# Optimization experiments

Hardware: AMD Instinct MI355X
Metric: run time of the kernel (lower is better)

## Reference

```python
import jax, jax.numpy as jnp
import numpy as np

B, L, K, D, S = 8, 1024, 1024, 128, 16  # batch, nodes, eigvecs, d_model(=d_inner), d_state
ABAR_EPS = 1e-3
BN_EPS = 1e-5


def setup_inputs() -> dict:
    key = jax.random.key(0)
    ks = jax.random.split(key, 10)
    x = jax.random.normal(ks[0], (B, L, D), jnp.float32)
    attn_mask = jnp.ones((B, L), jnp.bool_)
    EigVecs = jax.random.normal(ks[1], (B, L, K), jnp.float32)
    EigVals = jax.random.uniform(ks[2], (B, K), jnp.float32)
    # BatchNorm1d (eval mode) params
    bn_gamma = jnp.ones((D,), jnp.float32)
    bn_beta = jnp.zeros((D,), jnp.float32)
    bn_mean = jnp.zeros((D,), jnp.float32)
    bn_var = jnp.ones((D,), jnp.float32)
    # in_proj Linear(D, 2*D)
    W_in = jax.random.normal(ks[3], (D, 2 * D), jnp.float32) / np.float32(np.sqrt(D))
    b_in = jnp.zeros((2 * D,), jnp.float32)
    # SSM params
    log_Delta = np.float32(np.log(1e-3)) + np.float32(np.log(0.1) - np.log(1e-3)) * jax.random.uniform(ks[4], (1, D), jnp.float32)
    Bp = 0.01 * jax.random.normal(ks[5], (1, D, S), jnp.float32)
    Cp = 0.01 * jax.random.normal(ks[6], (1, D, S), jnp.float32)
    log_A_real = jnp.log(0.5 * jnp.ones((D, S), jnp.float32))
    A_imag = jnp.pi * jnp.broadcast_to(jnp.arange(D, dtype=jnp.float32)[:, None], (D, S))
    # out_proj Linear(D, D)
    W_out = jax.random.normal(ks[7], (D, D), jnp.float32) / np.float32(np.sqrt(D))
    b_out = jnp.zeros((D,), jnp.float32)
    return {
        "x": x, "attn_mask": attn_mask, "EigVecs": EigVecs, "EigVals": EigVals,
        "bn_gamma": bn_gamma, "bn_beta": bn_beta, "bn_mean": bn_mean, "bn_var": bn_var,
        "W_in": W_in, "b_in": b_in, "log_Delta": log_Delta, "Bp": Bp, "Cp": Cp,
        "log_A_real": log_A_real, "A_imag": A_imag, "W_out": W_out, "b_out": b_out,
    }


def reference(x, attn_mask, EigVecs, EigVals, bn_gamma, bn_beta, bn_mean, bn_var,
              W_in, b_in, log_Delta, Bp, Cp, log_A_real, A_imag, W_out, b_out):
    # --- eig preprocessing ---
    ev = 1.0 - EigVals[:, :, None, None]            # (B,K,1,1)
    ev = jnp.nan_to_num(ev)
    Q = jnp.nan_to_num(EigVecs)                      # (B,L,K)
    Q = Q / jnp.linalg.norm(Q, axis=-1, keepdims=True)
    Q = jnp.nan_to_num(Q)
    # --- in_proj: BatchNorm1d (eval) + Linear ---
    xb = (x - bn_mean) * (bn_gamma / jnp.sqrt(bn_var + BN_EPS)) + bn_beta
    h = xb @ W_in + b_in                             # (B,L,2D)
    x1, z = jnp.split(h, 2, axis=-1)                 # split [d_model, d_model]
    u = x1 * jax.nn.silu(z)                          # (B,L,D)
    # --- discretized SSM params ---
    delta = jnp.exp(log_Delta)                       # (1,D)
    A = -jnp.exp(log_A_real) + 1j * A_imag           # (D,S) complex
    Abar = jnp.exp(-ABAR_EPS + delta[..., None] * A) # (1,D,S) complex
    Bbar = delta[..., None] * Bp                     # (1,D,S)
    # --- graph Fourier transform ---
    QTX = jnp.einsum('blk,bld->bkd', Q, u)           # (B,K,D)
    QTXB = QTX[..., None] * Bbar                     # (B,K,D,S)
    lamA = ev * Abar[:, None]                        # (B,K,D,S) complex
    lamQ = jnp.real(lamA / (1.0 - lamA) * QTXB)      # A_complex & not BC_complex -> .real
    # --- inverse transform + C reduction (fused) ---
    yssm = jnp.einsum('blk,bkds,ds->bld', Q, lamQ, Cp[0])  # (B,L,D)
    y = jax.nn.silu(yssm) @ W_out + b_out
    return y
```

## Files before the change

kernel.cpp:

```cpp
#include <hip/hip_runtime.h>
#include <math.h>

#define B_ 8
#define L_ 1024
#define K_ 1024
#define D_ 128
#define S_ 16
#define DS_ (D_ * S_)
#define NIT_ 16

typedef short bf16x8 __attribute__((ext_vector_type(8)));
typedef float f32x4 __attribute__((ext_vector_type(4)));
typedef __attribute__((address_space(1))) const unsigned int gu32;
typedef __attribute__((address_space(3))) unsigned int lu32;

__device__ inline unsigned short f2bf(float f) {
    unsigned int u = __float_as_uint(f);
    u = (u + 0x7fffu + ((u >> 16) & 1u)) >> 16;
    return (unsigned short)u;
}
__device__ inline float bf2f(unsigned short h) {
    return __uint_as_float(((unsigned int)h) << 16);
}

__device__ inline size_t bswz(int b, int c, int n) {
    return ((((size_t)b * 32 + (c >> 5)) * 4 + ((c >> 3) & 3)) * 128 + n) * 8;
}

__global__ __launch_bounds__(256) void k_pre(
    const float* __restrict__ E, const float* __restrict__ x,
    const float* __restrict__ g, const float* __restrict__ beta,
    const float* __restrict__ mean, const float* __restrict__ var,
    const float* __restrict__ W_in, const float* __restrict__ b_in,
    const float* __restrict__ log_Delta, const float* __restrict__ Bp,
    const float* __restrict__ Cp, const float* __restrict__ log_A_real,
    const float* __restrict__ A_imag,
    float* __restrict__ rn_out, float* __restrict__ par,
    unsigned short* __restrict__ uswH, unsigned short* __restrict__ uswL) {
    __shared__ float xb[16][128];
    __shared__ float rsum[16];
    __shared__ float rnS[16];
    int bx = blockIdx.x;
    int row0 = bx * 16;
    int t = threadIdx.x;
    if (bx < 8) {
        int i = bx * 256 + t;
        int d = i >> 4, s = i & 15;
        double delta = exp((double)log_Delta[d]);
        double Are = -exp((double)log_A_real[i]);
        double Aim = (double)A_imag[i];
        double mag = exp(-1e-3 + delta * Are);
        double ang = delta * Aim;
        int o = s * D_ + d;
        par[o]           = (float)(mag * cos(ang));
        par[DS_ + o]     = (float)(mag * sin(ang));
        par[2 * DS_ + o] = (float)(delta * (double)Bp[i] * (double)Cp[i]);
    }
    {
        int r = t >> 4, tt = t & 15;
        const float4* Ep = (const float4*)(E + (size_t)(row0 + r) * K_);
        float s = 0.f;
        #pragma unroll
        for (int i = 0; i < 16; ++i) {
            float4 v = Ep[tt + i * 16];
            s += v.x * v.x + v.y * v.y + v.z * v.z + v.w * v.w;
        }
        s += __shfl_xor(s, 8, 64);
        s += __shfl_xor(s, 4, 64);
        s += __shfl_xor(s, 2, 64);
        s += __shfl_xor(s, 1, 64);
        if (tt == 0) rsum[r] = s;
    }
    #pragma unroll
    for (int p = 0; p < 8; ++p) {
        int idx = t + p * 256;
        int dd = idx & 127, r = idx >> 7;
        float sc = g[dd] / sqrtf(var[dd] + 1e-5f);
        xb[r][dd] = (x[(size_t)(row0 + r) * D_ + dd] - mean[dd]) * sc + beta[dd];
    }
    __syncthreads();
    if (t < 16) {
        float rv = 1.0f / sqrtf(rsum[t]);
        rnS[t] = rv;
        rn_out[row0 + t] = rv;
    }
    __syncthreads();
    int j = t & 127, half = t >> 7;
    float acc1[8], acc2[8];
    #pragma unroll
    for (int r = 0; r < 8; ++r) { acc1[r] = 0.f; acc2[r] = 0.f; }
    #pragma unroll 4
    for (int dd = 0; dd < 128; ++dd) {
        float w1 = W_in[dd * 256 + j];
        float w2 = W_in[dd * 256 + 128 + j];
        #pragma unroll
        for (int r = 0; r < 8; ++r) {
            float xv = xb[half * 8 + r][dd];
            acc1[r] = fmaf(xv, w1, acc1[r]);
            acc2[r] = fmaf(xv, w2, acc2[r]);
        }
    }
    float b1 = b_in[j], b2 = b_in[128 + j];
    bf16x8 hv, lv;
    #pragma unroll
    for (int r = 0; r < 8; ++r) {
        int rr = half * 8 + r;
        float x1 = acc1[r] + b1;
        float z  = acc2[r] + b2;
        float sig = 1.0f / (1.0f + __expf(-z));
        float uv = rnS[rr] * x1 * z * sig;
        unsigned short h = f2bf(uv);
        hv[r] = (short)h;
        lv[r] = (short)f2bf(uv - bf2f(h));
    }
    int b = row0 >> 10;
    int l0 = (row0 & 1023) + half * 8;
    size_t off = bswz(b, l0, j);
    *(bf16x8*)&uswH[off] = hv;
    *(bf16x8*)&uswL[off] = lv;
}

__global__ __launch_bounds__(256) void k_g1(
    const float* __restrict__ E,
    const unsigned short* __restrict__ BH, const unsigned short* __restrict__ BL,
    const float* __restrict__ EigVals, const float* __restrict__ par,
    unsigned short* __restrict__ GswH, unsigned short* __restrict__ GswL) {
    __shared__ unsigned short sAh[2][640], sAl[2][640];
    __shared__ unsigned short sBh[2][4128], sBl[2][4128];
    __shared__ float evS[16];
    __shared__ float Gs[16][132];
    int bx = blockIdx.x;
    int b = bx & 7;
    int m0 = (bx >> 3) * 16;
    const float* Ab = E + (size_t)b * (1024 * 1024);
    const unsigned short* BbH = BH + (size_t)b * 131072;
    const unsigned short* BbL = BL + (size_t)b * 131072;
    int t = threadIdx.x;
    int wave = t >> 6, lane = t & 63;
    int fr = lane & 15, q = lane >> 4;
    int wn = wave * 32;
    int am = t & 15, jj = t >> 4;
    int ag = jj >> 2;
    int arot = (ag + (am >> 3)) & 3;
    int aoff = am * 40 + arot * 8 + ((2 * jj) & 7);
    if (t < 16) evS[t] = 1.0f - EigVals[b * 1024 + m0 + t];
    f32x4 acc[2];
    acc[0] = (f32x4){0.f, 0.f, 0.f, 0.f};
    acc[1] = (f32x4){0.f, 0.f, 0.f, 0.f};

    for (int it = 0; it < NIT_; ++it) {
        int cb = it * 64;
        float v0 = Ab[(size_t)(cb + 2 * jj) * 1024 + m0 + am];
        float v1 = Ab[(size_t)(cb + 2 * jj + 1) * 1024 + m0 + am];
        float v2 = Ab[(size_t)(cb + 32 + 2 * jj) * 1024 + m0 + am];
        float v3 = Ab[(size_t)(cb + 32 + 2 * jj + 1) * 1024 + m0 + am];
        #pragma unroll
        for (int j2 = 0; j2 < 8; ++j2) {
            int s = wave + j2 * 4;
            int cts = s >> 4, s2 = s & 15;
            int qq = s2 & 3, nh = (s2 >> 2) & 1, hl = s2 >> 3;
            size_t src0 = (size_t)(it * 2 + cts) * 4096;
            const unsigned short* src =
                (hl ? BbL : BbH) + src0 + ((size_t)qq * 128 + nh * 64 + lane) * 8;
            unsigned short* dst = (hl ? sBl[cts] : sBh[cts]) + qq * 1032 + nh * 512;
            __builtin_amdgcn_global_load_lds((gu32*)src, (lu32*)dst, 16, 0, 0);
        }
        {
            unsigned short h0 = f2bf(v0), h1 = f2bf(v1);
            unsigned short l0 = f2bf(v0 - bf2f(h0)), l1 = f2bf(v1 - bf2f(h1));
            *(unsigned int*)&sAh[0][aoff] = (unsigned)h0 | ((unsigned)h1 << 16);
            *(unsigned int*)&sAl[0][aoff] = (unsigned)l0 | ((unsigned)l1 << 16);
            unsigned short h2 = f2bf(v2), h3 = f2bf(v3);
            unsigned short l2 = f2bf(v2 - bf2f(h2)), l3 = f2bf(v3 - bf2f(h3));
            *(unsigned int*)&sAh[1][aoff] = (unsigned)h2 | ((unsigned)h3 << 16);
            *(unsigned int*)&sAl[1][aoff] = (unsigned)l2 | ((unsigned)l3 << 16);
        }
        __syncthreads();
        #pragma unroll
        for (int ks = 0; ks < 2; ++ks) {
            bf16x8 ah, al, bh[2], bl[2];
            {
                int p = (q + (fr >> 3)) & 3;
                int off = fr * 40 + p * 8;
                ah = *(const bf16x8*)&sAh[ks][off];
                al = *(const bf16x8*)&sAl[ks][off];
            }
            #pragma unroll
            for (int nt = 0; nt < 2; ++nt) {
                int off = q * 1032 + (wn + nt * 16 + fr) * 8;
                bh[nt] = *(const bf16x8*)&sBh[ks][off];
                bl[nt] = *(const bf16x8*)&sBl[ks][off];
            }
            #pragma unroll
            for (int nt = 0; nt < 2; ++nt) {
                acc[nt] = __builtin_amdgcn_mfma_f32_16x16x32_bf16(ah, bh[nt], acc[nt], 0, 0, 0);
                acc[nt] = __builtin_amdgcn_mfma_f32_16x16x32_bf16(ah, bl[nt], acc[nt], 0, 0, 0);
                acc[nt] = __builtin_amdgcn_mfma_f32_16x16x32_bf16(al, bh[nt], acc[nt], 0, 0, 0);
            }
        }
        __syncthreads();
    }
    #pragma unroll
    for (int nt = 0; nt < 2; ++nt) {
        int col = wn + nt * 16 + fr;
        #pragma unroll
        for (int r = 0; r < 4; ++r)
            Gs[q * 4 + r][col] = acc[nt][r];
    }
    __syncthreads();
    {
        int col = t & 127, rowg = t >> 7;
        float arr[S_], aii[S_], ccc[S_];
        #pragma unroll
        for (int ss = 0; ss < S_; ++ss) {
            arr[ss] = par[ss * D_ + col];
            aii[ss] = par[DS_ + ss * D_ + col];
            ccc[ss] = par[2 * DS_ + ss * D_ + col];
        }
        #pragma unroll
        for (int i = 0; i < 8; ++i) {
            int row = rowg * 8 + i;
            float ev = evS[row];
            float w = 0.f;
            #pragma unroll
            for (int ss = 0; ss < S_; ++ss) {
                float a = ev * arr[ss], bi = ev * aii[ss];
                float oma = 1.0f - a;
                float b2 = bi * bi;
                float num = fmaf(a, oma, -b2);
                float den = fmaf(oma, oma, b2);
                float rr = __builtin_amdgcn_rcpf(den);
                rr = rr * (2.0f - den * rr);
                w = fmaf(ccc[ss], num * rr, w);
            }
            Gs[row][col] *= w;
        }
    }
    __syncthreads();
    {
        int d = t & 127, kg = t >> 7;
        bf16x8 hv, lv;
        #pragma unroll
        for (int i = 0; i < 8; ++i) {
            float v = Gs[kg * 8 + i][d];
            unsigned short h = f2bf(v);
            hv[i] = (short)h;
            lv[i] = (short)f2bf(v - bf2f(h));
        }
        int ct = m0 >> 5;
        int qsel = ((m0 >> 3) & 2) + kg;
        size_t off = (((size_t)(b * 32 + ct) * 4 + qsel) * 128 + d) * 8;
        *(bf16x8*)&GswH[off] = hv;
        *(bf16x8*)&GswL[off] = lv;
    }
}

__global__ __launch_bounds__(256) void k_g2(
    const float* __restrict__ E,
    const unsigned short* __restrict__ BH, const unsigned short* __restrict__ BL,
    const float* __restrict__ rn, const float* __restrict__ W_out,
    const float* __restrict__ b_out, float* __restrict__ y) {
    __shared__ unsigned short sAh[2][640], sAl[2][640];
    __shared__ unsigned short sBh[2][4128], sBl[2][4128];
    __shared__ float Ys[16][132];
    __shared__ float rnS[16];
    int bx = blockIdx.x;
    int b = bx & 7;
    int m0 = (bx >> 3) * 16;
    const float* Ab = E + (size_t)b * (1024 * 1024);
    const unsigned short* BbH = BH + (size_t)b * 131072;
    const unsigned short* BbL = BL + (size_t)b * 131072;
    int t = threadIdx.x;
    int wave = t >> 6, lane = t & 63;
    int fr = lane & 15, q = lane >> 4;
    int wn = wave * 32;
    int am = t >> 4, c4 = (t & 15) * 4;
    int chunk = c4 >> 5, cw = c4 & 31;
    int ag = cw >> 3;
    int arot = (ag + (am >> 3)) & 3;
    int aoff = am * 40 + arot * 8 + (cw & 7);
    if (t < 16) rnS[t] = rn[b * 1024 + m0 + t];
    f32x4 acc[2];
    acc[0] = (f32x4){0.f, 0.f, 0.f, 0.f};
    acc[1] = (f32x4){0.f, 0.f, 0.f, 0.f};

    for (int it = 0; it < NIT_; ++it) {
        int cb = it * 64;
        float4 va = *(const float4*)&Ab[(size_t)(m0 + am) * 1024 + cb + c4];
        #pragma unroll
        for (int j2 = 0; j2 < 8; ++j2) {
            int s = wave + j2 * 4;
            int cts = s >> 4, s2 = s & 15;
            int qq = s2 & 3, nh = (s2 >> 2) & 1, hl = s2 >> 3;
            size_t src0 = (size_t)(it * 2 + cts) * 4096;
            const unsigned short* src =
                (hl ? BbL : BbH) + src0 + ((size_t)qq * 128 + nh * 64 + lane) * 8;
            unsigned short* dst = (hl ? sBl[cts] : sBh[cts]) + qq * 1032 + nh * 512;
            __builtin_amdgcn_global_load_lds((gu32*)src, (lu32*)dst, 16, 0, 0);
        }
        {
            unsigned short h0 = f2bf(va.x), h1 = f2bf(va.y);
            unsigned short h2 = f2bf(va.z), h3 = f2bf(va.w);
            unsigned short l0 = f2bf(va.x - bf2f(h0)), l1 = f2bf(va.y - bf2f(h1));
            unsigned short l2 = f2bf(va.z - bf2f(h2)), l3 = f2bf(va.w - bf2f(h3));
            *(uint2*)&sAh[chunk][aoff] =
                (uint2){(unsigned)h0 | ((unsigned)h1 << 16),
                        (unsigned)h2 | ((unsigned)h3 << 16)};
            *(uint2*)&sAl[chunk][aoff] =
                (uint2){(unsigned)l0 | ((unsigned)l1 << 16),
                        (unsigned)l2 | ((unsigned)l3 << 16)};
        }
        __syncthreads();
        #pragma unroll
        for (int ks = 0; ks < 2; ++ks) {
            bf16x8 ah, al, bh[2], bl[2];
            {
                int p = (q + (fr >> 3)) & 3;
                int off = fr * 40 + p * 8;
                ah = *(const bf16x8*)&sAh[ks][off];
                al = *(const bf16x8*)&sAl[ks][off];
            }
            #pragma unroll
            for (int nt = 0; nt < 2; ++nt) {
                int off = q * 1032 + (wn + nt * 16 + fr) * 8;
                bh[nt] = *(const bf16x8*)&sBh[ks][off];
                bl[nt] = *(const bf16x8*)&sBl[ks][off];
            }
            #pragma unroll
            for (int nt = 0; nt < 2; ++nt) {
                acc[nt] = __builtin_amdgcn_mfma_f32_16x16x32_bf16(ah, bh[nt], acc[nt], 0, 0, 0);
                acc[nt] = __builtin_amdgcn_mfma_f32_16x16x32_bf16(ah, bl[nt], acc[nt], 0, 0, 0);
                acc[nt] = __builtin_amdgcn_mfma_f32_16x16x32_bf16(al, bh[nt], acc[nt], 0, 0, 0);
            }
        }
        __syncthreads();
    }
    #pragma unroll
    for (int nt = 0; nt < 2; ++nt) {
        int col = wn + nt * 16 + fr;
        #pragma unroll
        for (int r = 0; r < 4; ++r) {
            int row = q * 4 + r;
            float v = acc[nt][r] * rnS[row];
            float sig = 1.0f / (1.0f + __expf(-v));
            Ys[row][col] = v * sig;
        }
    }
    __syncthreads();
    int j = t & 127, h = t >> 7;
    float a2[8];
    #pragma unroll
    for (int r = 0; r < 8; ++r) a2[r] = 0.f;
    for (int dd = 0; dd < 128; dd += 4) {
        float w0 = W_out[(dd + 0) * 128 + j];
        float w1 = W_out[(dd + 1) * 128 + j];
        float w2 = W_out[(dd + 2) * 128 + j];
        float w3 = W_out[(dd + 3) * 128 + j];
        #pragma unroll
        for (int r = 0; r < 8; ++r) {
            float4 yv = *(float4*)&Ys[h * 8 + r][dd];
            a2[r] = fmaf(yv.x, w0, a2[r]);
            a2[r] = fmaf(yv.y, w1, a2[r]);
            a2[r] = fmaf(yv.z, w2, a2[r]);
            a2[r] = fmaf(yv.w, w3, a2[r]);
        }
    }
    float bo = b_out[j];
    #pragma unroll
    for (int r = 0; r < 8; ++r)
        y[((size_t)b * 1024 + m0 + h * 8 + r) * 128 + j] = a2[r] + bo;
}

extern "C" void kernel_launch(void* const* d_in, const int* in_sizes, int n_in,
                              void* d_out, int out_size, void* d_ws, size_t ws_size,
                              hipStream_t stream) {
    const float* x          = (const float*)d_in[0];
    const float* EigVecs    = (const float*)d_in[2];
    const float* EigVals    = (const float*)d_in[3];
    const float* bn_gamma   = (const float*)d_in[4];
    const float* bn_beta    = (const float*)d_in[5];
    const float* bn_mean    = (const float*)d_in[6];
    const float* bn_var     = (const float*)d_in[7];
    const float* W_in       = (const float*)d_in[8];
    const float* b_in       = (const float*)d_in[9];
    const float* log_Delta  = (const float*)d_in[10];
    const float* Bp         = (const float*)d_in[11];
    const float* Cp         = (const float*)d_in[12];
    const float* log_A_real = (const float*)d_in[13];
    const float* A_imag     = (const float*)d_in[14];
    const float* W_out      = (const float*)d_in[15];
    const float* b_out      = (const float*)d_in[16];

    float* y = (float*)d_out;
    char* w = (char*)d_ws;
    float* rn            = (float*)(w);
    float* par           = (float*)(w + 32768);
    unsigned short* uswH = (unsigned short*)(w + 65536);
    unsigned short* uswL = (unsigned short*)(w + 65536 + (1u << 21));
    unsigned short* GswH = (unsigned short*)(w + 65536 + 2 * (1u << 21));
    unsigned short* GswL = (unsigned short*)(w + 65536 + 3 * (1u << 21));

    k_pre<<<dim3(B_ * L_ / 16), dim3(256), 0, stream>>>(
        EigVecs, x, bn_gamma, bn_beta, bn_mean, bn_var, W_in, b_in,
        log_Delta, Bp, Cp, log_A_real, A_imag, rn, par, uswH, uswL);
    k_g1<<<dim3(512), dim3(256), 0, stream>>>(
        EigVecs, uswH, uswL, EigVals, par, GswH, GswL);
    k_g2<<<dim3(512), dim3(256), 0, stream>>>(
        EigVecs, GswH, GswL, rn, W_out, b_out, y);
}
```

Before: 172.2 us.

## Double-buffer LDS tiles in k_g1/k_g2 to overlap loads with MFMA

Both split-bf16 GEMM kernels now keep two LDS buffers for the A and B tiles. The next iteration's global loads and global_load_lds copies are issued before the current tile's MFMAs, and each iteration ends with a single waitcnt plus barrier instead of two __syncthreads. s_setprio is raised around the MFMA section, and the epilogue scratch (Gs/Ys) now aliases the B buffer, which offsets the extra LDS. The intent is to hide global latency behind compute, at the cost of double the tile LDS footprint and therefore possibly lower occupancy.

Measured after the change: 167.8 us. 2.6% less time.

```diff
diff --git a/kernel.cpp b/kernel.cpp
--- a/kernel.cpp
+++ b/kernel.cpp
@@ -120,15 +120,40 @@
     *(bf16x8*)&uswL[off] = lv;
 }
 
+#define STAGE_B(itS, nb)                                                        \
+    _Pragma("unroll")                                                           \
+    for (int j2 = 0; j2 < 8; ++j2) {                                            \
+        int s = wave + j2 * 4;                                      \
+        int cts = s >> 4, s2 = s & 15;                                          \
+        int qq = s2 & 3, nh = (s2 >> 2) & 1, hl = s2 >> 3;                      \
+        size_t src0 = (size_t)((itS) * 2 + cts) * 4096;                         \
+        const unsigned short* src =                                             \
+            (hl ? BbL : BbH) + src0 + ((size_t)qq * 128 + nh * 64 + lane) * 8;  \
+        unsigned short* dst =                                                   \
+            (hl ? &sBl[nb][cts][0] : &sBh[nb][cts][0]) + qq * 1032 + nh * 512;  \
+        __builtin_amdgcn_global_load_lds((gu32*)src, (lu32*)dst, 16, 0, 0);     \
+    }
+
+#define G1_WRITE_A(nb, v0, v1, v2, v3)                                           \
+    {                                                                            \
+        unsigned short h0 = f2bf(v0), h1 = f2bf(v1);                             \
+        unsigned short l0 = f2bf((v0) - bf2f(h0)), l1 = f2bf((v1) - bf2f(h1));   \
+        *(unsigned int*)&sAh[nb][0][aoff] = (unsigned)h0 | ((unsigned)h1 << 16); \
+        *(unsigned int*)&sAl[nb][0][aoff] = (unsigned)l0 | ((unsigned)l1 << 16); \
+        unsigned short h2 = f2bf(v2), h3 = f2bf(v3);                             \
+        unsigned short l2 = f2bf((v2) - bf2f(h2)), l3 = f2bf((v3) - bf2f(h3));   \
+        *(unsigned int*)&sAh[nb][1][aoff] = (unsigned)h2 | ((unsigned)h3 << 16); \
+        *(unsigned int*)&sAl[nb][1][aoff] = (unsigned)l2 | ((unsigned)l3 << 16); \
+    }
+
 __global__ __launch_bounds__(256) void k_g1(
     const float* __restrict__ E,
     const unsigned short* __restrict__ BH, const unsigned short* __restrict__ BL,
     const float* __restrict__ EigVals, const float* __restrict__ par,
     unsigned short* __restrict__ GswH, unsigned short* __restrict__ GswL) {
-    __shared__ unsigned short sAh[2][640], sAl[2][640];
-    __shared__ unsigned short sBh[2][4128], sBl[2][4128];
+    __shared__ alignas(16) unsigned short sAh[2][2][640], sAl[2][2][640];
+    __shared__ alignas(16) unsigned short sBh[2][2][4128], sBl[2][2][4128];
     __shared__ float evS[16];
-    __shared__ float Gs[16][132];
     int bx = blockIdx.x;
     int b = bx & 7;
     int m0 = (bx >> 3) * 16;
@@ -148,48 +173,44 @@
     acc[0] = (f32x4){0.f, 0.f, 0.f, 0.f};
     acc[1] = (f32x4){0.f, 0.f, 0.f, 0.f};
 
+    {
+        float v0 = Ab[(size_t)(2 * jj) * 1024 + m0 + am];
+        float v1 = Ab[(size_t)(2 * jj + 1) * 1024 + m0 + am];
+        float v2 = Ab[(size_t)(32 + 2 * jj) * 1024 + m0 + am];
+        float v3 = Ab[(size_t)(32 + 2 * jj + 1) * 1024 + m0 + am];
+        STAGE_B(0, 0);
+        G1_WRITE_A(0, v0, v1, v2, v3);
+        asm volatile("s_waitcnt vmcnt(0) lgkmcnt(0)" ::: "memory");
+        __builtin_amdgcn_s_barrier();
+    }
+
+    #pragma unroll 2
     for (int it = 0; it < NIT_; ++it) {
-        int cb = it * 64;
-        float v0 = Ab[(size_t)(cb + 2 * jj) * 1024 + m0 + am];
-        float v1 = Ab[(size_t)(cb + 2 * jj + 1) * 1024 + m0 + am];
-        float v2 = Ab[(size_t)(cb + 32 + 2 * jj) * 1024 + m0 + am];
-        float v3 = Ab[(size_t)(cb + 32 + 2 * jj + 1) * 1024 + m0 + am];
-        #pragma unroll
-        for (int j2 = 0; j2 < 8; ++j2) {
-            int s = wave + j2 * 4;
-            int cts = s >> 4, s2 = s & 15;
-            int qq = s2 & 3, nh = (s2 >> 2) & 1, hl = s2 >> 3;
-            size_t src0 = (size_t)(it * 2 + cts) * 4096;
-            const unsigned short* src =
-                (hl ? BbL : BbH) + src0 + ((size_t)qq * 128 + nh * 64 + lane) * 8;
-            unsigned short* dst = (hl ? sBl[cts] : sBh[cts]) + qq * 1032 + nh * 512;
-            __builtin_amdgcn_global_load_lds((gu32*)src, (lu32*)dst, 16, 0, 0);
-        }
-        {
-            unsigned short h0 = f2bf(v0), h1 = f2bf(v1);
-            unsigned short l0 = f2bf(v0 - bf2f(h0)), l1 = f2bf(v1 - bf2f(h1));
-            *(unsigned int*)&sAh[0][aoff] = (unsigned)h0 | ((unsigned)h1 << 16);
-            *(unsigned int*)&sAl[0][aoff] = (unsigned)l0 | ((unsigned)l1 << 16);
-            unsigned short h2 = f2bf(v2), h3 = f2bf(v3);
-            unsigned short l2 = f2bf(v2 - bf2f(h2)), l3 = f2bf(v3 - bf2f(h3));
-            *(unsigned int*)&sAh[1][aoff] = (unsigned)h2 | ((unsigned)h3 << 16);
-            *(unsigned int*)&sAl[1][aoff] = (unsigned)l2 | ((unsigned)l3 << 16);
-        }
-        __syncthreads();
+        int buf = it & 1, nb = buf ^ 1;
+        float v0 = 0.f, v1 = 0.f, v2 = 0.f, v3 = 0.f;
+        if (it + 1 < NIT_) {
+            int cb = (it + 1) * 64;
+            v0 = Ab[(size_t)(cb + 2 * jj) * 1024 + m0 + am];
+            v1 = Ab[(size_t)(cb + 2 * jj + 1) * 1024 + m0 + am];
+            v2 = Ab[(size_t)(cb + 32 + 2 * jj) * 1024 + m0 + am];
+            v3 = Ab[(size_t)(cb + 32 + 2 * jj + 1) * 1024 + m0 + am];
+            STAGE_B(it + 1, nb);
+        }
+        __builtin_amdgcn_s_setprio(1);
         #pragma unroll
         for (int ks = 0; ks < 2; ++ks) {
             bf16x8 ah, al, bh[2], bl[2];
             {
                 int p = (q + (fr >> 3)) & 3;
                 int off = fr * 40 + p * 8;
-                ah = *(const bf16x8*)&sAh[ks][off];
-                al = *(const bf16x8*)&sAl[ks][off];
+                ah = *(const bf16x8*)&sAh[buf][ks][off];
+                al = *(const bf16x8*)&sAl[buf][ks][off];
             }
             #pragma unroll
             for (int nt = 0; nt < 2; ++nt) {
                 int off = q * 1032 + (wn + nt * 16 + fr) * 8;
-                bh[nt] = *(const bf16x8*)&sBh[ks][off];
-                bl[nt] = *(const bf16x8*)&sBl[ks][off];
+                bh[nt] = *(const bf16x8*)&sBh[buf][ks][off];
+                bl[nt] = *(const bf16x8*)&sBl[buf][ks][off];
             }
             #pragma unroll
             for (int nt = 0; nt < 2; ++nt) {
@@ -198,8 +219,13 @@
                 acc[nt] = __builtin_amdgcn_mfma_f32_16x16x32_bf16(al, bh[nt], acc[nt], 0, 0, 0);
             }
         }
-        __syncthreads();
-    }
+        __builtin_amdgcn_s_setprio(0);
+        if (it + 1 < NIT_) G1_WRITE_A(nb, v0, v1, v2, v3);
+        asm volatile("s_waitcnt vmcnt(0) lgkmcnt(0)" ::: "memory");
+        __builtin_amdgcn_s_barrier();
+    }
+
+    float (*Gs)[132] = (float (*)[132])(&sBh[0][0][0]);
     #pragma unroll
     for (int nt = 0; nt < 2; ++nt) {
         int col = wn + nt * 16 + fr;
@@ -260,9 +286,8 @@
     const unsigned short* __restrict__ BH, const unsigned short* __restrict__ BL,
     const float* __restrict__ rn, const float* __restrict__ W_out,
     const float* __restrict__ b_out, float* __restrict__ y) {
-    __shared__ unsigned short sAh[2][640], sAl[2][640];
-    __shared__ unsigned short sBh[2][4128], sBl[2][4128];
-    __shared__ float Ys[16][132];
+    __shared__ alignas(16) unsigned short sAh[2][2][640], sAl[2][2][640];
+    __shared__ alignas(16) unsigned short sBh[2][2][4128], sBl[2][2][4128];
     __shared__ float rnS[16];
     int bx = blockIdx.x;
     int b = bx & 7;
@@ -284,47 +309,52 @@
     acc[0] = (f32x4){0.f, 0.f, 0.f, 0.f};
     acc[1] = (f32x4){0.f, 0.f, 0.f, 0.f};
 
+#define G2_WRITE_A(nb, va)                                                       \
+    {                                                                            \
+        unsigned short h0 = f2bf((va).x), h1 = f2bf((va).y);                     \
+        unsigned short h2 = f2bf((va).z), h3 = f2bf((va).w);                     \
+        unsigned short l0 = f2bf((va).x - bf2f(h0)), l1 = f2bf((va).y - bf2f(h1));\
+        unsigned short l2 = f2bf((va).z - bf2f(h2)), l3 = f2bf((va).w - bf2f(h3));\
+        *(uint2*)&sAh[nb][chunk][aoff] =                                         \
+            (uint2){(unsigned)h0 | ((unsigned)h1 << 16),                         \
+                    (unsigned)h2 | ((unsigned)h3 << 16)};                        \
+        *(uint2*)&sAl[nb][chunk][aoff] =                                         \
+            (uint2){(unsigned)l0 | ((unsigned)l1 << 16),                         \
+                    (unsigned)l2 | ((unsigned)l3 << 16)};                        \
+    }
+
+    {
+        float4 va = *(const float4*)&Ab[(size_t)(m0 + am) * 1024 + c4];
+        STAGE_B(0, 0);
+        G2_WRITE_A(0, va);
+        asm volatile("s_waitcnt vmcnt(0) lgkmcnt(0)" ::: "memory");
+        __builtin_amdgcn_s_barrier();
+    }
+
+    #pragma unroll 2
     for (int it = 0; it < NIT_; ++it) {
-        int cb = it * 64;
-        float4 va = *(const float4*)&Ab[(size_t)(m0 + am) * 1024 + cb + c4];
-        #pragma unroll
-        for (int j2 = 0; j2 < 8; ++j2) {
-            int s = wave + j2 * 4;
-            int cts = s >> 4, s2 = s & 15;
-            int qq = s2 & 3, nh = (s2 >> 2) & 1, hl = s2 >> 3;
-            size_t src0 = (size_t)(it * 2 + cts) * 4096;
-            const unsigned short* src =
-                (hl ? BbL : BbH) + src0 + ((size_t)qq * 128 + nh * 64 + lane) * 8;
-            unsigned short* dst = (hl ? sBl[cts] : sBh[cts]) + qq * 1032 + nh * 512;
-            __builtin_amdgcn_global_load_lds((gu32*)src, (lu32*)dst, 16, 0, 0);
-        }
-        {
-            unsigned short h0 = f2bf(va.x), h1 = f2bf(va.y);
-            unsigned short h2 = f2bf(va.z), h3 = f2bf(va.w);
-            unsigned short l0 = f2bf(va.x - bf2f(h0)), l1 = f2bf(va.y - bf2f(h1));
-            unsigned short l2 = f2bf(va.z - bf2f(h2)), l3 = f2bf(va.w - bf2f(h3));
-            *(uint2*)&sAh[chunk][aoff] =
-                (uint2){(unsigned)h0 | ((unsigned)h1 << 16),
-                        (unsigned)h2 | ((unsigned)h3 << 16)};
-            *(uint2*)&sAl[chunk][aoff] =
-                (uint2){(unsigned)l0 | ((unsigned)l1 << 16),
-                        (unsigned)l2 | ((unsigned)l3 << 16)};
-        }
-        __syncthreads();
+        int buf = it & 1, nb = buf ^ 1;
+        float4 va = (float4){0.f, 0.f, 0.f, 0.f};
+        if (it + 1 < NIT_) {
+            int cb = (it + 1) * 64;
+            va = *(const float4*)&Ab[(size_t)(m0 + am) * 1024 + cb + c4];
+            STAGE_B(it + 1, nb);
+        }
+        __builtin_amdgcn_s_setprio(1);
         #pragma unroll
         for (int ks = 0; ks < 2; ++ks) {
             bf16x8 ah, al, bh[2], bl[2];
             {
                 int p = (q + (fr >> 3)) & 3;
                 int off = fr * 40 + p * 8;
-                ah = *(const bf16x8*)&sAh[ks][off];
-                al = *(const bf16x8*)&sAl[ks][off];
+                ah = *(const bf16x8*)&sAh[buf][ks][off];
+                al = *(const bf16x8*)&sAl[buf][ks][off];
             }
             #pragma unroll
             for (int nt = 0; nt < 2; ++nt) {
                 int off = q * 1032 + (wn + nt * 16 + fr) * 8;
-                bh[nt] = *(const bf16x8*)&sBh[ks][off];
-                bl[nt] = *(const bf16x8*)&sBl[ks][off];
+                bh[nt] = *(const bf16x8*)&sBh[buf][ks][off];
+                bl[nt] = *(const bf16x8*)&sBl[buf][ks][off];
             }
             #pragma unroll
             for (int nt = 0; nt < 2; ++nt) {
@@ -333,8 +363,13 @@
                 acc[nt] = __builtin_amdgcn_mfma_f32_16x16x32_bf16(al, bh[nt], acc[nt], 0, 0, 0);
             }
         }
-        __syncthreads();
-    }
+        __builtin_amdgcn_s_setprio(0);
+        if (it + 1 < NIT_) G2_WRITE_A(nb, va);
+        asm volatile("s_waitcnt vmcnt(0) lgkmcnt(0)" ::: "memory");
+        __builtin_amdgcn_s_barrier();
+    }
+
+    float (*Ys)[132] = (float (*)[132])(&sBh[0][0][0]);
     #pragma unroll
     for (int nt = 0; nt < 2; ++nt) {
         int col = wn + nt * 16 + fr;
```

## Load GEMM fragments directly into registers with double-buffered software pipelining

Applied to the files above, without the earlier changes.

Both GEMM kernels drop the LDS staging of A and B tiles and the per-iteration barriers. Each lane now loads its own MFMA fragments straight from global memory into registers, using a two-stage register double buffer so the next tile's loads and bf16 split overlap the current tile's MFMAs. MFMA sections are wrapped in s_setprio, and launch bounds request 2 blocks per SM. In exchange, k_g1 now reads the A tile with strided, uncoalesced column loads (a 1024-float stride per row), B fragments are fetched redundantly by several waves with no LDS sharing, and register pressure rises.

Result: slower. 177.2 us (+2.9%).

```diff
diff --git a/kernel.cpp b/kernel.cpp
--- a/kernel.cpp
+++ b/kernel.cpp
@@ -11,8 +11,6 @@
 
 typedef short bf16x8 __attribute__((ext_vector_type(8)));
 typedef float f32x4 __attribute__((ext_vector_type(4)));
-typedef __attribute__((address_space(1))) const unsigned int gu32;
-typedef __attribute__((address_space(3))) unsigned int lu32;
 
 __device__ inline unsigned short f2bf(float f) {
     unsigned int u = __float_as_uint(f);
@@ -120,86 +118,95 @@
     *(bf16x8*)&uswL[off] = lv;
 }
 
-__global__ __launch_bounds__(256) void k_g1(
+
+#define G1_LOADA(tl)                                                     \
+    _Pragma("unroll")                                                    \
+    for (int i = 0; i < 8; ++i) {                                        \
+        rawA[i]     = Acol[(size_t)((tl) * 64 + q * 8 + i) * 1024];      \
+        rawA[i + 8] = Acol[(size_t)((tl) * 64 + 32 + q * 8 + i) * 1024]; \
+    }
+
+#define LOADB(S, tl)                                                     \
+    _Pragma("unroll")                                                    \
+    for (int ks = 0; ks < 2; ++ks) {                                     \
+        size_t base = ((size_t)((tl) * 2 + ks) * 4 + q) * 128;           \
+        _Pragma("unroll")                                                \
+        for (int nt = 0; nt < 2; ++nt) {                                 \
+            bh##S[ks][nt] = pBH[base + wn + nt * 16 + fr];               \
+            bl##S[ks][nt] = pBL[base + wn + nt * 16 + fr];               \
+        }                                                                \
+    }
+
+#define CONVA(S)                                                         \
+    _Pragma("unroll")                                                    \
+    for (int ks = 0; ks < 2; ++ks)                                       \
+        _Pragma("unroll")                                                \
+        for (int i = 0; i < 8; ++i) {                                    \
+            float v = rawA[ks * 8 + i];                                  \
+            unsigned short h = f2bf(v);                                  \
+            ah##S[ks][i] = (short)h;                                     \
+            al##S[ks][i] = (short)f2bf(v - bf2f(h));                     \
+        }
+
+#define MFMA_ON(S)                                                       \
+    __builtin_amdgcn_s_setprio(1);                                       \
+    _Pragma("unroll")                                                    \
+    for (int ks = 0; ks < 2; ++ks)                                       \
+        _Pragma("unroll")                                                \
+        for (int nt = 0; nt < 2; ++nt) {                                 \
+            acc[nt] = __builtin_amdgcn_mfma_f32_16x16x32_bf16(ah##S[ks], bh##S[ks][nt], acc[nt], 0, 0, 0); \
+            acc[nt] = __builtin_amdgcn_mfma_f32_16x16x32_bf16(ah##S[ks], bl##S[ks][nt], acc[nt], 0, 0, 0); \
+            acc[nt] = __builtin_amdgcn_mfma_f32_16x16x32_bf16(al##S[ks], bh##S[ks][nt], acc[nt], 0, 0, 0); \
+        }                                                                \
+    __builtin_amdgcn_s_setprio(0);
+
+#define FRAG_DECLS                                                       \
+    bf16x8 ah0[2], al0[2], bh0[2][2], bl0[2][2];                         \
+    bf16x8 ah1[2], al1[2], bh1[2][2], bl1[2][2];                         \
+    float rawA[16];
+
+__global__ __launch_bounds__(256, 2) void k_g1(
     const float* __restrict__ E,
     const unsigned short* __restrict__ BH, const unsigned short* __restrict__ BL,
     const float* __restrict__ EigVals, const float* __restrict__ par,
     unsigned short* __restrict__ GswH, unsigned short* __restrict__ GswL) {
-    __shared__ unsigned short sAh[2][640], sAl[2][640];
-    __shared__ unsigned short sBh[2][4128], sBl[2][4128];
     __shared__ float evS[16];
     __shared__ float Gs[16][132];
     int bx = blockIdx.x;
     int b = bx & 7;
     int m0 = (bx >> 3) * 16;
     const float* Ab = E + (size_t)b * (1024 * 1024);
-    const unsigned short* BbH = BH + (size_t)b * 131072;
-    const unsigned short* BbL = BL + (size_t)b * 131072;
+    const bf16x8* pBH = (const bf16x8*)(BH + (size_t)b * 131072);
+    const bf16x8* pBL = (const bf16x8*)(BL + (size_t)b * 131072);
     int t = threadIdx.x;
     int wave = t >> 6, lane = t & 63;
     int fr = lane & 15, q = lane >> 4;
     int wn = wave * 32;
-    int am = t & 15, jj = t >> 4;
-    int ag = jj >> 2;
-    int arot = (ag + (am >> 3)) & 3;
-    int aoff = am * 40 + arot * 8 + ((2 * jj) & 7);
+    const float* Acol = Ab + m0 + fr;
     if (t < 16) evS[t] = 1.0f - EigVals[b * 1024 + m0 + t];
+    __syncthreads();
+    FRAG_DECLS
     f32x4 acc[2];
     acc[0] = (f32x4){0.f, 0.f, 0.f, 0.f};
     acc[1] = (f32x4){0.f, 0.f, 0.f, 0.f};
 
-    for (int it = 0; it < NIT_; ++it) {
-        int cb = it * 64;
-        float v0 = Ab[(size_t)(cb + 2 * jj) * 1024 + m0 + am];
-        float v1 = Ab[(size_t)(cb + 2 * jj + 1) * 1024 + m0 + am];
-        float v2 = Ab[(size_t)(cb + 32 + 2 * jj) * 1024 + m0 + am];
-        float v3 = Ab[(size_t)(cb + 32 + 2 * jj + 1) * 1024 + m0 + am];
-        #pragma unroll
-        for (int j2 = 0; j2 < 8; ++j2) {
-            int s = wave + j2 * 4;
-            int cts = s >> 4, s2 = s & 15;
-            int qq = s2 & 3, nh = (s2 >> 2) & 1, hl = s2 >> 3;
-            size_t src0 = (size_t)(it * 2 + cts) * 4096;
-            const unsigned short* src =
-                (hl ? BbL : BbH) + src0 + ((size_t)qq * 128 + nh * 64 + lane) * 8;
-            unsigned short* dst = (hl ? sBl[cts] : sBh[cts]) + qq * 1032 + nh * 512;
-            __builtin_amdgcn_global_load_lds((gu32*)src, (lu32*)dst, 16, 0, 0);
-        }
+    G1_LOADA(0); LOADB(0, 0); CONVA(0);
+
+    for (int it = 0; it < NIT_; it += 2) {
         {
-            unsigned short h0 = f2bf(v0), h1 = f2bf(v1);
-            unsigned short l0 = f2bf(v0 - bf2f(h0)), l1 = f2bf(v1 - bf2f(h1));
-            *(unsigned int*)&sAh[0][aoff] = (unsigned)h0 | ((unsigned)h1 << 16);
-            *(unsigned int*)&sAl[0][aoff] = (unsigned)l0 | ((unsigned)l1 << 16);
-            unsigned short h2 = f2bf(v2), h3 = f2bf(v3);
-            unsigned short l2 = f2bf(v2 - bf2f(h2)), l3 = f2bf(v3 - bf2f(h3));
-            *(unsigned int*)&sAh[1][aoff] = (unsigned)h2 | ((unsigned)h3 << 16);
-            *(unsigned int*)&sAl[1][aoff] = (unsigned)l2 | ((unsigned)l3 << 16);
-        }
-        __syncthreads();
-        #pragma unroll
-        for (int ks = 0; ks < 2; ++ks) {
-            bf16x8 ah, al, bh[2], bl[2];
-            {
-                int p = (q + (fr >> 3)) & 3;
-                int off = fr * 40 + p * 8;
-                ah = *(const bf16x8*)&sAh[ks][off];
-                al = *(const bf16x8*)&sAl[ks][off];
-            }
-            #pragma unroll
-            for (int nt = 0; nt < 2; ++nt) {
-                int off = q * 1032 + (wn + nt * 16 + fr) * 8;
-                bh[nt] = *(const bf16x8*)&sBh[ks][off];
-                bl[nt] = *(const bf16x8*)&sBl[ks][off];
-            }
-            #pragma unroll
-            for (int nt = 0; nt < 2; ++nt) {
-                acc[nt] = __builtin_amdgcn_mfma_f32_16x16x32_bf16(ah, bh[nt], acc[nt], 0, 0, 0);
-                acc[nt] = __builtin_amdgcn_mfma_f32_16x16x32_bf16(ah, bl[nt], acc[nt], 0, 0, 0);
-                acc[nt] = __builtin_amdgcn_mfma_f32_16x16x32_bf16(al, bh[nt], acc[nt], 0, 0, 0);
-            }
-        }
-        __syncthreads();
-    }
+            int tl = it + 1;
+            G1_LOADA(tl); LOADB(1, tl);
+            MFMA_ON(0);
+            CONVA(1);
+        }
+        {
+            int tl = (it + 2 < NIT_) ? it + 2 : 0;
+            G1_LOADA(tl); LOADB(0, tl);
+            MFMA_ON(1);
+            CONVA(0);
+        }
+    }
+
     #pragma unroll
     for (int nt = 0; nt < 2; ++nt) {
         int col = wn + nt * 16 + fr;
@@ -255,86 +262,78 @@
     }
 }
 
-__global__ __launch_bounds__(256) void k_g2(
+#define G2_LOADA(tl)                                                     \
+    _Pragma("unroll")                                                    \
+    for (int ks = 0; ks < 2; ++ks) {                                     \
+        rA0[ks] = *(const float4*)&Arow[(tl) * 64 + ks * 32 + q * 8];    \
+        rA1[ks] = *(const float4*)&Arow[(tl) * 64 + ks * 32 + q * 8 + 4];\
+    }
+
+#define G2_CONVA(S)                                                      \
+    _Pragma("unroll")                                                    \
+    for (int ks = 0; ks < 2; ++ks) {                                     \
+        float vv0 = rA0[ks].x, vv1 = rA0[ks].y, vv2 = rA0[ks].z, vv3 = rA0[ks].w; \
+        float vv4 = rA1[ks].x, vv5 = rA1[ks].y, vv6 = rA1[ks].z, vv7 = rA1[ks].w; \
+        unsigned short h0 = f2bf(vv0), h1 = f2bf(vv1), h2 = f2bf(vv2), h3 = f2bf(vv3); \
+        unsigned short h4 = f2bf(vv4), h5 = f2bf(vv5), h6 = f2bf(vv6), h7 = f2bf(vv7); \
+        ah##S[ks][0] = (short)h0; ah##S[ks][1] = (short)h1;              \
+        ah##S[ks][2] = (short)h2; ah##S[ks][3] = (short)h3;              \
+        ah##S[ks][4] = (short)h4; ah##S[ks][5] = (short)h5;              \
+        ah##S[ks][6] = (short)h6; ah##S[ks][7] = (short)h7;              \
+        al##S[ks][0] = (short)f2bf(vv0 - bf2f(h0));                      \
+        al##S[ks][1] = (short)f2bf(vv1 - bf2f(h1));                      \
+        al##S[ks][2] = (short)f2bf(vv2 - bf2f(h2));                      \
+        al##S[ks][3] = (short)f2bf(vv3 - bf2f(h3));                      \
+        al##S[ks][4] = (short)f2bf(vv4 - bf2f(h4));                      \
+        al##S[ks][5] = (short)f2bf(vv5 - bf2f(h5));                      \
+        al##S[ks][6] = (short)f2bf(vv6 - bf2f(h6));                      \
+        al##S[ks][7] = (short)f2bf(vv7 - bf2f(h7));                      \
+    }
+
+__global__ __launch_bounds__(256, 2) void k_g2(
     const float* __restrict__ E,
     const unsigned short* __restrict__ BH, const unsigned short* __restrict__ BL,
     const float* __restrict__ rn, const float* __restrict__ W_out,
     const float* __restrict__ b_out, float* __restrict__ y) {
-    __shared__ unsigned short sAh[2][640], sAl[2][640];
-    __shared__ unsigned short sBh[2][4128], sBl[2][4128];
     __shared__ float Ys[16][132];
     __shared__ float rnS[16];
     int bx = blockIdx.x;
     int b = bx & 7;
     int m0 = (bx >> 3) * 16;
     const float* Ab = E + (size_t)b * (1024 * 1024);
-    const unsigned short* BbH = BH + (size_t)b * 131072;
-    const unsigned short* BbL = BL + (size_t)b * 131072;
+    const bf16x8* pBH = (const bf16x8*)(BH + (size_t)b * 131072);
+    const bf16x8* pBL = (const bf16x8*)(BL + (size_t)b * 131072);
     int t = threadIdx.x;
     int wave = t >> 6, lane = t & 63;
     int fr = lane & 15, q = lane >> 4;
     int wn = wave * 32;
-    int am = t >> 4, c4 = (t & 15) * 4;
-    int chunk = c4 >> 5, cw = c4 & 31;
-    int ag = cw >> 3;
-    int arot = (ag + (am >> 3)) & 3;
-    int aoff = am * 40 + arot * 8 + (cw & 7);
+    const float* Arow = Ab + (size_t)(m0 + fr) * 1024;
     if (t < 16) rnS[t] = rn[b * 1024 + m0 + t];
+    __syncthreads();
+    bf16x8 ah0[2], al0[2], bh0[2][2], bl0[2][2];
+    bf16x8 ah1[2], al1[2], bh1[2][2], bl1[2][2];
+    float4 rA0[2], rA1[2];
     f32x4 acc[2];
     acc[0] = (f32x4){0.f, 0.f, 0.f, 0.f};
     acc[1] = (f32x4){0.f, 0.f, 0.f, 0.f};
 
-    for (int it = 0; it < NIT_; ++it) {
-        int cb = it * 64;
-        float4 va = *(const float4*)&Ab[(size_t)(m0 + am) * 1024 + cb + c4];
-        #pragma unroll
-        for (int j2 = 0; j2 < 8; ++j2) {
-            int s = wave + j2 * 4;
-            int cts = s >> 4, s2 = s & 15;
-            int qq = s2 & 3, nh = (s2 >> 2) & 1, hl = s2 >> 3;
-            size_t src0 = (size_t)(it * 2 + cts) * 4096;
-            const unsigned short* src =
-                (hl ? BbL : BbH) + src0 + ((size_t)qq * 128 + nh * 64 + lane) * 8;
-            unsigned short* dst = (hl ? sBl[cts] : sBh[cts]) + qq * 1032 + nh * 512;
-            __builtin_amdgcn_global_load_lds((gu32*)src, (lu32*)dst, 16, 0, 0);
-        }
+    G2_LOADA(0); LOADB(0, 0); G2_CONVA(0);
+
+    for (int it = 0; it < NIT_; it += 2) {
         {
-            unsigned short h0 = f2bf(va.x), h1 = f2bf(va.y);
-            unsigned short h2 = f2bf(va.z), h3 = f2bf(va.w);
-            unsigned short l0 = f2bf(va.x - bf2f(h0)), l1 = f2bf(va.y - bf2f(h1));
-            unsigned short l2 = f2bf(va.z - bf2f(h2)), l3 = f2bf(va.w - bf2f(h3));
-            *(uint2*)&sAh[chunk][aoff] =
-                (uint2){(unsigned)h0 | ((unsigned)h1 << 16),
-                        (unsigned)h2 | ((unsigned)h3 << 16)};
-            *(uint2*)&sAl[chunk][aoff] =
-                (uint2){(unsigned)l0 | ((unsigned)l1 << 16),
-                        (unsigned)l2 | ((unsigned)l3 << 16)};
-        }
-        __syncthreads();
-        #pragma unroll
-        for (int ks = 0; ks < 2; ++ks) {
-            bf16x8 ah, al, bh[2], bl[2];
-            {
-                int p = (q + (fr >> 3)) & 3;
-                int off = fr * 40 + p * 8;
-                ah = *(const bf16x8*)&sAh[ks][off];
-                al = *(const bf16x8*)&sAl[ks][off];
-            }
-            #pragma unroll
-            for (int nt = 0; nt < 2; ++nt) {
-                int off = q * 1032 + (wn + nt * 16 + fr) * 8;
-                bh[nt] = *(const bf16x8*)&sBh[ks][off];
-                bl[nt] = *(const bf16x8*)&sBl[ks][off];
-            }
-            #pragma unroll
-            for (int nt = 0; nt < 2; ++nt) {
-                acc[nt] = __builtin_amdgcn_mfma_f32_16x16x32_bf16(ah, bh[nt], acc[nt], 0, 0, 0);
-                acc[nt] = __builtin_amdgcn_mfma_f32_16x16x32_bf16(ah, bl[nt], acc[nt], 0, 0, 0);
-                acc[nt] = __builtin_amdgcn_mfma_f32_16x16x32_bf16(al, bh[nt], acc[nt], 0, 0, 0);
-            }
-        }
-        __syncthreads();
-    }
+            int tl = it + 1;
+            G2_LOADA(tl); LOADB(1, tl);
+            MFMA_ON(0);
+            G2_CONVA(1);
+        }
+        {
+            int tl = (it + 2 < NIT_) ? it + 2 : 0;
+            G2_LOADA(tl); LOADB(0, tl);
+            MFMA_ON(1);
+            G2_CONVA(0);
+        }
+    }
+
     #pragma unroll
     for (int nt = 0; nt < 2; ++nt) {
         int col = wn + nt * 16 + fr;
```
